# Performance work log

Measured on AMD Instinct MI355X. Metric: run time of the kernel, lower is better.

## Reference

```python
import jax, jax.numpy as jnp
import numpy as np

# ---- static config (from module code / init_kwargs) ----
D_MODEL = 512
D_STATE = 64
D_CONV = 4
EXPAND = 2
HEADDIM = 64
D_INNER = EXPAND * D_MODEL          # 1024
NHEADS = D_INNER // HEADDIM         # 16
D_IN_PROJ = 2 * D_INNER + 2 * D_STATE + NHEADS  # 2192
CONV_DIM = D_INNER + 2 * D_STATE    # 1152
N_LAYERS = 2
VOCAB = 32768
BATCH = 2
SEQ = 512
EPS = 1e-5


def setup_inputs() -> dict:
    key = jax.random.key(0)
    ks = jax.random.split(key, 12)
    g = lambda k, shape, s=0.02: (jax.random.normal(k, shape, jnp.float32) * s)
    return {
        "input_ids": jax.random.randint(ks[0], (BATCH, SEQ), 0, VOCAB),
        "padding_mask": jnp.zeros((BATCH, SEQ), dtype=bool),  # True = pad
        "embeddings": g(ks[1], (VOCAB, D_MODEL)),
        "in_proj_w": g(ks[2], (N_LAYERS, D_IN_PROJ, D_MODEL)),
        "conv_w": g(ks[3], (N_LAYERS, CONV_DIM, D_CONV), 0.1),
        "conv_b": jnp.zeros((N_LAYERS, CONV_DIM), jnp.float32),
        "dt_bias": g(ks[4], (N_LAYERS, NHEADS), 0.5),
        "A_log": jnp.log(jax.random.uniform(ks[5], (N_LAYERS, NHEADS), jnp.float32, 1.0, 16.0)),
        "D_ssm": jnp.ones((N_LAYERS, NHEADS), jnp.float32),
        "norm_w": jnp.ones((N_LAYERS, D_INNER), jnp.float32),
        "out_proj_w": g(ks[6], (N_LAYERS, D_MODEL, D_INNER)),
        "aggr_w": g(ks[7], (D_MODEL, 2 * D_MODEL)),
        "aggr_b": jnp.zeros((D_MODEL,), jnp.float32),
        "norm_f_w": jnp.ones((D_MODEL,), jnp.float32),
        "lm_head_w": g(ks[8], (VOCAB, D_MODEL)),
        "lm_head_b": jnp.zeros((VOCAB,), jnp.float32),
    }


def rmsnorm(x, w):
    return x * jax.lax.rsqrt(jnp.mean(x * x, axis=-1, keepdims=True) + EPS) * w


def flip_sc(X, padding_mask):
    # reverse the valid (non-pad) prefix of each sequence, leave pad positions in place
    b, l, _ = X.shape
    lengths = jnp.sum(~padding_mask, axis=1)                        # (b,)
    pos = jnp.arange(l)[None, :]                                    # (1,l)
    keep = pos < lengths[:, None]
    rev = jnp.where(keep, lengths[:, None] - 1 - pos, pos)          # (b,l)
    return jnp.take_along_axis(X, rev[:, :, None], axis=1)


def causal_conv(x, w, b):
    # x: (b,l,c); depthwise causal conv with kernel size D_CONV
    xt = jnp.transpose(x, (0, 2, 1))                                # (b,c,l)
    y = jax.lax.conv_general_dilated(
        xt, w[:, None, :], window_strides=(1,), padding=[(D_CONV - 1, 0)],
        feature_group_count=w.shape[0], dimension_numbers=("NCH", "OIH", "NCH"))
    return jnp.transpose(y + b[None, :, None], (0, 2, 1))


def ssd_scan(x, dt, A, B, C):
    # x:(b,l,h,p) dt:(b,l,h) A:(h,) B,C:(b,l,n) -> y:(b,l,h,p)
    bsz = x.shape[0]
    dA = jnp.exp(dt * A)                                            # (b,l,h)
    dtx = dt[..., None] * x                                         # (b,l,h,p)
    def step(h, inp):
        dA_t, dtx_t, B_t, C_t = inp
        h = h * dA_t[:, :, None, None] + dtx_t[..., None] * B_t[:, None, None, :]
        y = jnp.einsum("bhpn,bn->bhp", h, C_t)
        return h, y
    h0 = jnp.zeros((bsz, NHEADS, HEADDIM, D_STATE), x.dtype)
    xs = (jnp.swapaxes(dA, 0, 1), jnp.swapaxes(dtx, 0, 1),
          jnp.swapaxes(B, 0, 1), jnp.swapaxes(C, 0, 1))
    _, ys = jax.lax.scan(step, h0, xs)
    return jnp.swapaxes(ys, 0, 1)


def mamba2_block(x, wi, cw, cb, dtb, alog, dss, nw, wo):
    # Mamba2 layer with residual (EncoderLayer: mamba(X) + X)
    b, l, _ = x.shape
    zxbcdt = jnp.einsum("bld,ed->ble", x, wi)                      # (b,l,D_IN_PROJ)
    z = zxbcdt[..., :D_INNER]
    xBC = zxbcdt[..., D_INNER:D_INNER + CONV_DIM]
    dt = jax.nn.softplus(zxbcdt[..., D_INNER + CONV_DIM:] + dtb)   # (b,l,h)
    xBC = jax.nn.silu(causal_conv(xBC, cw, cb))
    xs = xBC[..., :D_INNER].reshape(b, l, NHEADS, HEADDIM)
    B = xBC[..., D_INNER:D_INNER + D_STATE]
    C = xBC[..., D_INNER + D_STATE:]
    A = -jnp.exp(alog)                                             # (h,)
    y = ssd_scan(xs, dt, A, B, C) + xs * dss[None, None, :, None]
    y = y.reshape(b, l, D_INNER)
    y = rmsnorm(y * jax.nn.silu(z), nw)                            # RMSNormGated
    return jnp.einsum("ble,de->bld", y, wo) + x


def reference(input_ids, padding_mask, embeddings, in_proj_w, conv_w, conv_b,
              dt_bias, A_log, D_ssm, norm_w, out_proj_w, aggr_w, aggr_b,
              norm_f_w, lm_head_w, lm_head_b):
    X = embeddings[input_ids]                                      # (b,l,d)
    for i in range(N_LAYERS):
        X_flip = flip_sc(X, padding_mask)
        X_f = mamba2_block(X, in_proj_w[i], conv_w[i], conv_b[i], dt_bias[i],
                           A_log[i], D_ssm[i], norm_w[i], out_proj_w[i])
        X_b = mamba2_block(X_flip, in_proj_w[i], conv_w[i], conv_b[i], dt_bias[i],
                           A_log[i], D_ssm[i], norm_w[i], out_proj_w[i])
        X_b = flip_sc(X_b, padding_mask)
        # gated bidirectional fusion
        zg = jax.nn.sigmoid(jnp.concatenate([X_f, X_b], axis=-1) @ aggr_w.T + aggr_b)
        X = zg * X_f + (1.0 - zg) * X_b
    h = rmsnorm(X, norm_f_w)
    logits = h @ lm_head_w.T + lm_head_b                            # (b,l,V)
    return logits
```

## Files before the change

kernel.cpp:

```cpp
#include <hip/hip_runtime.h>

#define SEQ    512
#define DM     512
#define DI     1024
#define NH     16
#define DS     64
#define CONVD  1152
#define DPROJ  2192
#define NPADIN 2304

typedef __attribute__((ext_vector_type(8))) short bf16x8;
typedef __attribute__((ext_vector_type(4))) float floatx4;

__device__ __forceinline__ unsigned int f2bf(float f) {
  unsigned int u = __float_as_uint(f);
  u += 0x7FFFu + ((u >> 16) & 1u);
  return u >> 16;
}
__device__ __forceinline__ ushort4 cvt4(float4 v) {
  ushort4 o;
  o.x = (unsigned short)f2bf(v.x); o.y = (unsigned short)f2bf(v.y);
  o.z = (unsigned short)f2bf(v.z); o.w = (unsigned short)f2bf(v.w);
  return o;
}
__device__ __forceinline__ float sigmoidf_(float x) { return 1.f / (1.f + __expf(-x)); }
__device__ __forceinline__ float siluf_(float x) { return x * sigmoidf_(x); }

__device__ __forceinline__ void gl16(const void* g, void* l) {
  __builtin_amdgcn_global_load_lds(
      (const __attribute__((address_space(1))) unsigned int*)g,
      (__attribute__((address_space(3))) unsigned int*)l, 16, 0, 0);
}

template<int BM, int BN, int EPI>
__global__ __launch_bounds__(256) void gemm_bf(
    const short* __restrict__ A, const short* __restrict__ B,
    float* __restrict__ C, const int K, const int Nvalid, const int ldc,
    const float* __restrict__ e0, const float* __restrict__ e1,
    unsigned short* __restrict__ o2)
{
  constexpr int FM = BM / 32, FN = BN / 32;
  constexpr int PA = BM / 32, PB = BN / 32;
  __shared__ short As[BM * 64];
  __shared__ short Bs[BN * 64];
  const int tid = threadIdx.x, lane = tid & 63, wave = tid >> 6;
  const int m0 = blockIdx.y * BM, n0 = blockIdx.x * BN;
  const int wm = (wave >> 1) * (BM / 2), wn = (wave & 1) * (BN / 2);
  const int prow = wave * 8 + (lane >> 3);
  const int schk = ((lane & 7) ^ (prow & 7)) << 3;
  const short* agp = A + (size_t)(m0 + prow) * K + schk;
  const short* bgp = B + (size_t)(n0 + prow) * K + schk;
  short* albase = &As[wave * 8 * 64];
  short* blbase = &Bs[wave * 8 * 64];
  const int r16 = lane & 15, quad = lane >> 4;

  floatx4 acc[FM][FN];
#pragma unroll
  for (int i = 0; i < FM; i++)
#pragma unroll
    for (int j = 0; j < FN; j++) acc[i][j] = (floatx4)0.f;

  for (int k0 = 0; k0 < K; k0 += 64) {
#pragma unroll
    for (int p = 0; p < PA; ++p)
      gl16(agp + (size_t)p * 32 * K + k0, albase + p * 32 * 64);
#pragma unroll
    for (int p = 0; p < PB; ++p)
      gl16(bgp + (size_t)p * 32 * K + k0, blbase + p * 32 * 64);
    __syncthreads();
#pragma unroll
    for (int kk = 0; kk < 2; ++kk) {
      bf16x8 afr[FM], bfr[FN];
#pragma unroll
      for (int i = 0; i < FM; i++) {
        const int row = wm + i * 16 + r16;
        afr[i] = *(const bf16x8*)&As[row * 64 + (((kk * 4 + quad) ^ (row & 7)) << 3)];
      }
#pragma unroll
      for (int j = 0; j < FN; j++) {
        const int row = wn + j * 16 + r16;
        bfr[j] = *(const bf16x8*)&Bs[row * 64 + (((kk * 4 + quad) ^ (row & 7)) << 3)];
      }
#pragma unroll
      for (int i = 0; i < FM; i++)
#pragma unroll
        for (int j = 0; j < FN; j++)
          acc[i][j] = __builtin_amdgcn_mfma_f32_16x16x32_bf16(afr[i], bfr[j], acc[i][j], 0, 0, 0);
    }
    __syncthreads();
  }

  const int er = quad << 2;
#pragma unroll
  for (int i = 0; i < FM; ++i)
#pragma unroll
    for (int j = 0; j < FN; ++j)
#pragma unroll
      for (int r = 0; r < 4; ++r) {
        const int gm = m0 + wm + i * 16 + er + r;
        const int gn = n0 + wn + j * 16 + r16;
        float v = acc[i][j][r];
        if (EPI == 0) {
          if (gn < Nvalid) C[(size_t)gm * ldc + gn] = v;
        } else if (EPI == 1) {
          const int mm = gm & 1023;
          v += e0[(size_t)mm * DM + gn];
          const size_t idx = (size_t)mm * DI + ((gm >> 10) << 9) + gn;
          C[idx] = v;
          o2[idx] = (unsigned short)f2bf(v);
        } else if (EPI == 2) {
          const float zg = sigmoidf_(v + e0[gn]);
          const float xn = zg * e1[(size_t)gm * DI + gn] +
                           (1.f - zg) * e1[(size_t)gm * DI + DM + gn];
          const size_t idx = (size_t)gm * DM + gn;
          C[idx] = xn;
          o2[idx] = (unsigned short)f2bf(xn);
        } else {
          C[(size_t)gm * ldc + gn] = v + e0[gn];
        }
      }
}

#define WO4  262144
#define AW4  131072
#define LM4  4194304
__global__ __launch_bounds__(256) void prep_k(
    const int* __restrict__ ids, const float* __restrict__ emb,
    const float* __restrict__ wi, const float* __restrict__ wo,
    const float* __restrict__ aw, const float* __restrict__ lmw,
    float* __restrict__ Xf, unsigned short* __restrict__ Xb,
    unsigned short* __restrict__ wiB, unsigned short* __restrict__ woB,
    unsigned short* __restrict__ awB, unsigned short* __restrict__ lmwB) {
  const int blk = blockIdx.x, tid = threadIdx.x;
  if (blk < 512) {
    const int m = blk * 2 + (tid >> 7), col = tid & 127;
    const int row = ids[m];
    float4 v = ((const float4*)(emb + (size_t)row * DM))[col];
    ((float4*)(Xf + (size_t)m * DM))[col] = v;
    ((ushort4*)(Xb + (size_t)m * DM))[col] = cvt4(v);
  } else if (blk < 512 + 2304) {
    const int slot = (blk - 512) * 2 + (tid >> 7), col = tid & 127;
    const int l = slot >= 2304 ? 1 : 0;
    const int row = slot - l * 2304;
    ushort4 o; o.x = o.y = o.z = o.w = 0;
    if (row < DPROJ)
      o = cvt4(((const float4*)(wi + ((size_t)l * DPROJ + row) * DM))[col]);
    ((ushort4*)(wiB + ((size_t)l * NPADIN + row) * DM))[col] = o;
  } else {
    for (int i = (blk - 2816) * 256 + tid; i < WO4 + AW4 + LM4; i += 4480 * 256) {
      int j = i;
      const float4* s; ushort4* d;
      if (j < WO4)            { s = (const float4*)wo;  d = (ushort4*)woB; }
      else if (j < WO4 + AW4) { j -= WO4; s = (const float4*)aw;  d = (ushort4*)awB; }
      else                    { j -= WO4 + AW4; s = (const float4*)lmw; d = (ushort4*)lmwB; }
      d[j] = cvt4(s[j]);
    }
  }
}

__global__ __launch_bounds__(256) void conv_k(const float* __restrict__ zx,
    const float* __restrict__ cw, const float* __restrict__ cb,
    const float* __restrict__ dtb, const float* __restrict__ alog,
    float* __restrict__ xact, float* __restrict__ dtt, float* __restrict__ dAt) {
  const int t0 = (blockIdx.x & 31) << 4;
  const int half = blockIdx.x >> 5;
  const int b = blockIdx.y;
  const float* src = zx + (size_t)b * SEQ * DPROJ + DI;
  float* d0 = xact + (size_t)b * SEQ * CONVD;
  float* d1 = xact + (size_t)(2 + b) * SEQ * CONVD;

  for (int cc = 0; cc < 3; ++cc) {
    const int ci = cc * 256 + threadIdx.x;
    if (ci >= 576) break;
    const int c = half * 576 + ci;
    const float w0 = cw[c*4+0], w1 = cw[c*4+1], w2 = cw[c*4+2], w3 = cw[c*4+3];
    const float bias = cb[c];
    float a_[22];
#pragma unroll
    for (int j = 0; j < 22; ++j) {
      const int t = t0 - 3 + j;
      a_[j] = (t >= 0 && t < SEQ) ? src[(size_t)t * DPROJ + c] : 0.f;
    }
#pragma unroll
    for (int tt = 0; tt < 16; ++tt) {
      const float f = bias + w0*a_[tt]   + w1*a_[tt+1] + w2*a_[tt+2] + w3*a_[tt+3];
      const float g = bias + w3*a_[tt+3] + w2*a_[tt+4] + w1*a_[tt+5] + w0*a_[tt+6];
      d0[(size_t)(t0+tt) * CONVD + c] = siluf_(f);
      d1[(size_t)(t0+tt) * CONVD + c] = siluf_(g);
    }
  }
  if (half == 0) {
    const int hh = threadIdx.x >> 4, tt2 = threadIdx.x & 15;
    const int t = t0 + tt2;
    const float v = zx[(size_t)(b * SEQ + t) * DPROJ + 2176 + hh] + dtb[hh];
    const float dt = (v > 15.f) ? v : log1pf(__expf(v));
    const float A = -__expf(alog[hh]);
    dtt[(b * NH + hh) * SEQ + t] = dt;
    dAt[(b * NH + hh) * SEQ + t] = __expf(dt * A);
  }
}

__global__ __launch_bounds__(256, 1) void scan_k(const float* __restrict__ xact,
    const float* __restrict__ dtt, const float* __restrict__ dAt,
    float* __restrict__ yn) {
  const int bid = blockIdx.x;
  const int dir = bid >> 7, b = (bid >> 6) & 1, h = (bid >> 2) & 15;
  const int ph = (bid >> 1) & 1, nh = bid & 1;
  const int tid = threadIdx.x, pl = tid & 31, nq = tid >> 5;
  const int p = ph * 32 + pl, nb = nq << 2;
  const float* __restrict__ src = xact + (size_t)(dir * 2 + b) * SEQ * CONVD;
  const float* __restrict__ dtp = dtt + (b * NH + h) * SEQ;
  const float* __restrict__ dap = dAt + (b * NH + h) * SEQ;
  float* __restrict__ yrow = yn + (size_t)nh * (4 * SEQ * DI)
      + (size_t)(dir * 2 + b) * SEQ * DI + h * 64 + ph * 32;
  __shared__ float yp[2][8][16][33];
  float hs[4] = {0.f, 0.f, 0.f, 0.f};
  int pb = 0;

  for (int c0 = 0; c0 < SEQ; c0 += 16, pb ^= 1) {
#pragma unroll
    for (int s = 0; s < 16; ++s) {
      const int tn = dir ? (SEQ - 1 - (c0 + s)) : (c0 + s);
      const float* row = src + (size_t)tn * CONVD;
      const float dts = dtp[tn];
      const float das = dap[tn];
      const float xv = row[h * 64 + p];
      const float4 b4 = *(const float4*)(row + DI + nh * 32 + nb);
      const float4 c4 = *(const float4*)(row + DI + DS + nh * 32 + nb);
      const float dtx = dts * xv;
      float ya;
      hs[0] = hs[0] * das + dtx * b4.x; ya  = hs[0] * c4.x;
      hs[1] = hs[1] * das + dtx * b4.y; ya += hs[1] * c4.y;
      hs[2] = hs[2] * das + dtx * b4.z; ya += hs[2] * c4.z;
      hs[3] = hs[3] * das + dtx * b4.w; ya += hs[3] * c4.w;
      yp[pb][nq][s][pl] = ya;
    }
    __syncthreads();
    {
      const int rt = tid >> 4, rp = (tid & 15) << 1;
      const int tn = dir ? (SEQ - 1 - (c0 + rt)) : (c0 + rt);
      float s0 = 0.f, s1 = 0.f;
#pragma unroll
      for (int j = 0; j < 8; ++j) { s0 += yp[pb][j][rt][rp]; s1 += yp[pb][j][rt][rp + 1]; }
      float2 o; o.x = s0; o.y = s1;
      *(float2*)&yrow[(size_t)tn * DI + rp] = o;
    }
  }
}

__global__ __launch_bounds__(256) void p2_k(const float* __restrict__ yn,
    const float* __restrict__ xact, const float* __restrict__ zx,
    const float* __restrict__ dss, const float* __restrict__ nw,
    unsigned short* __restrict__ A2b) {
  const int m2 = blockIdx.x;
  const int e4 = threadIdx.x << 2;
  const float4 ya = *(const float4*)(yn + (size_t)m2 * DI + e4);
  const float4 yb = *(const float4*)(yn + (size_t)4 * SEQ * DI + (size_t)m2 * DI + e4);
  const float4 x4 = *(const float4*)(xact + (size_t)m2 * CONVD + e4);
  const float4 z4 = *(const float4*)(zx + (size_t)(m2 & 1023) * DPROJ + e4);
  const float d = dss[e4 >> 6];
  float4 g;
  g.x = (ya.x + yb.x + x4.x * d) * siluf_(z4.x);
  g.y = (ya.y + yb.y + x4.y * d) * siluf_(z4.y);
  g.z = (ya.z + yb.z + x4.z * d) * siluf_(z4.z);
  g.w = (ya.w + yb.w + x4.w * d) * siluf_(z4.w);
  float ss = g.x*g.x + g.y*g.y + g.z*g.z + g.w*g.w;
#pragma unroll
  for (int m = 32; m >= 1; m >>= 1) ss += __shfl_xor(ss, m);
  __shared__ float red[4];
  if ((threadIdx.x & 63) == 0) red[threadIdx.x >> 6] = ss;
  __syncthreads();
  const float tot = red[0] + red[1] + red[2] + red[3];
  const float sc = rsqrtf(tot * (1.f / 1024.f) + 1e-5f);
  const float4 w4 = *(const float4*)(nw + e4);
  float4 o;
  o.x = g.x * sc * w4.x; o.y = g.y * sc * w4.y;
  o.z = g.z * sc * w4.z; o.w = g.w * sc * w4.w;
  ((ushort4*)(A2b + (size_t)m2 * DI))[threadIdx.x] = cvt4(o);
}

__global__ __launch_bounds__(128) void fnorm_k(const float* __restrict__ X,
    const float* __restrict__ w, unsigned short* __restrict__ outb) {
  const int m = blockIdx.x;
  const int e4 = threadIdx.x << 2;
  const float4 x4 = *(const float4*)(X + (size_t)m * DM + e4);
  float ss = x4.x*x4.x + x4.y*x4.y + x4.z*x4.z + x4.w*x4.w;
#pragma unroll
  for (int mm = 32; mm >= 1; mm >>= 1) ss += __shfl_xor(ss, mm);
  __shared__ float red[2];
  if ((threadIdx.x & 63) == 0) red[threadIdx.x >> 6] = ss;
  __syncthreads();
  const float tot = red[0] + red[1];
  const float sc = rsqrtf(tot * (1.f / 512.f) + 1e-5f);
  const float4 w4 = *(const float4*)(w + e4);
  float4 o;
  o.x = x4.x * sc * w4.x; o.y = x4.y * sc * w4.y;
  o.z = x4.z * sc * w4.z; o.w = x4.w * sc * w4.w;
  ((ushort4*)(outb + (size_t)m * DM))[threadIdx.x] = cvt4(o);
}

extern "C" void kernel_launch(void* const* d_in, const int* in_sizes, int n_in,
                              void* d_out, int out_size, void* d_ws, size_t ws_size,
                              hipStream_t stream) {
  (void)in_sizes; (void)n_in; (void)out_size; (void)ws_size;
  const int*   ids  = (const int*)d_in[0];
  const float* emb  = (const float*)d_in[2];
  const float* wi   = (const float*)d_in[3];
  const float* cw   = (const float*)d_in[4];
  const float* cb   = (const float*)d_in[5];
  const float* dtb  = (const float*)d_in[6];
  const float* alog = (const float*)d_in[7];
  const float* dss  = (const float*)d_in[8];
  const float* nw   = (const float*)d_in[9];
  const float* wo   = (const float*)d_in[10];
  const float* aw   = (const float*)d_in[11];
  const float* ab   = (const float*)d_in[12];
  const float* nfw  = (const float*)d_in[13];
  const float* lmw  = (const float*)d_in[14];
  const float* lmb  = (const float*)d_in[15];
  float* out = (float*)d_out;

  float* ws    = (float*)d_ws;
  float* Xf    = ws;
  float* zx    = Xf    + (size_t)524288;
  float* xact  = zx    + (size_t)2244608;
  float* dtt   = xact  + (size_t)2359296;
  float* dAt   = dtt   + (size_t)16384;
  float* yn    = dAt   + (size_t)16384;
  float* Xcatf = yn    + (size_t)4194304;
  unsigned short* Xb    = (unsigned short*)(Xcatf + (size_t)1048576);
  unsigned short* A2b   = Xb    + (size_t)524288;
  unsigned short* Xcatb = A2b   + (size_t)2097152;
  unsigned short* hnb   = Xcatb + (size_t)1048576;
  unsigned short* wiB   = hnb   + (size_t)524288;
  unsigned short* woB   = wiB   + (size_t)2359296;
  unsigned short* awB   = woB   + (size_t)1048576;
  unsigned short* lmwB  = awB   + (size_t)524288;

  prep_k<<<dim3(7296), dim3(256), 0, stream>>>(ids, emb, wi, wo, aw, lmw,
                                               Xf, Xb, wiB, woB, awB, lmwB);

  for (int layer = 0; layer < 2; ++layer) {
    gemm_bf<128, 128, 0><<<dim3(18, 8), dim3(256), 0, stream>>>(
        (const short*)Xb, (const short*)(wiB + (size_t)layer * NPADIN * DM),
        zx, 512, 2192, 2192, nullptr, nullptr, nullptr);
    conv_k<<<dim3(64, 2), dim3(256), 0, stream>>>(
        zx, cw + (size_t)layer * 4608, cb + (size_t)layer * 1152,
        dtb + 16 * layer, alog + 16 * layer, xact, dtt, dAt);
    scan_k<<<dim3(256), dim3(256), 0, stream>>>(xact, dtt, dAt, yn);
    p2_k<<<dim3(2048), dim3(256), 0, stream>>>(yn, xact, zx, dss + 16 * layer,
                                               nw + (size_t)layer * 1024, A2b);
    gemm_bf<64, 128, 1><<<dim3(4, 32), dim3(256), 0, stream>>>(
        (const short*)A2b, (const short*)(woB + (size_t)layer * DM * DI),
        Xcatf, 1024, 512, 512, Xf, nullptr, Xcatb);
    gemm_bf<64, 64, 2><<<dim3(8, 16), dim3(256), 0, stream>>>(
        (const short*)Xcatb, (const short*)awB,
        Xf, 1024, 512, 512, ab, Xcatf, Xb);
  }
  fnorm_k<<<dim3(1024), dim3(128), 0, stream>>>(Xf, nfw, hnb);
  gemm_bf<128, 128, 3><<<dim3(256, 8), dim3(256), 0, stream>>>(
      (const short*)hnb, (const short*)lmwB, out, 512, 32768, 32768, lmb, nullptr, nullptr);
}
```

Baseline: 513.7 us.

## Fuse fp32-to-bf16 weight conversion into GEMM B-tile loads, drop weight prep pass

Removes the prep pass that converted all weights (in_proj, out_proj, aggr, lm_head) to bf16 copies in workspace. The GEMM now reads fp32 weight rows directly, converts them with packed bf16 conversion instructions, and stores them into the swizzled shared tile, clamping out-of-range rows instead of relying on zero padding. This avoids writing and re-reading a bf16 weight copy, but doubles the B-operand global read bytes and swaps async global-to-LDS loads for register-staged loads, which may reduce latency hiding, notably in the large lm_head GEMM where each weight tile is re-read by every M block.

After: 550.1 us. 7.1% more time.

```diff
diff --git a/kernel.cpp b/kernel.cpp
--- a/kernel.cpp
+++ b/kernel.cpp
@@ -7,7 +7,6 @@
 #define DS     64
 #define CONVD  1152
 #define DPROJ  2192
-#define NPADIN 2304
 
 typedef __attribute__((ext_vector_type(8))) short bf16x8;
 typedef __attribute__((ext_vector_type(4))) float floatx4;
@@ -23,6 +22,11 @@
   o.z = (unsigned short)f2bf(v.z); o.w = (unsigned short)f2bf(v.w);
   return o;
 }
+__device__ __forceinline__ unsigned int cvtpk(float lo, float hi) {
+  unsigned int r;
+  asm("v_cvt_pk_bf16_f32 %0, %1, %2" : "=v"(r) : "v"(lo), "v"(hi));
+  return r;
+}
 __device__ __forceinline__ float sigmoidf_(float x) { return 1.f / (1.f + __expf(-x)); }
 __device__ __forceinline__ float siluf_(float x) { return x * sigmoidf_(x); }
 
@@ -34,7 +38,7 @@
 
 template<int BM, int BN, int EPI>
 __global__ __launch_bounds__(256) void gemm_bf(
-    const short* __restrict__ A, const short* __restrict__ B,
+    const short* __restrict__ A, const float* __restrict__ B,
     float* __restrict__ C, const int K, const int Nvalid, const int ldc,
     const float* __restrict__ e0, const float* __restrict__ e1,
     unsigned short* __restrict__ o2)
@@ -49,9 +53,7 @@
   const int prow = wave * 8 + (lane >> 3);
   const int schk = ((lane & 7) ^ (prow & 7)) << 3;
   const short* agp = A + (size_t)(m0 + prow) * K + schk;
-  const short* bgp = B + (size_t)(n0 + prow) * K + schk;
   short* albase = &As[wave * 8 * 64];
-  short* blbase = &Bs[wave * 8 * 64];
   const int r16 = lane & 15, quad = lane >> 4;
 
   floatx4 acc[FM][FN];
@@ -65,8 +67,17 @@
     for (int p = 0; p < PA; ++p)
       gl16(agp + (size_t)p * 32 * K + k0, albase + p * 32 * 64);
 #pragma unroll
-    for (int p = 0; p < PB; ++p)
-      gl16(bgp + (size_t)p * 32 * K + k0, blbase + p * 32 * 64);
+    for (int p = 0; p < PB; ++p) {
+      int brow = n0 + p * 32 + prow;
+      brow = (brow < Nvalid) ? brow : (Nvalid - 1);
+      const float* src = B + (size_t)brow * K + k0 + schk;
+      const float4 f0 = *(const float4*)(src);
+      const float4 f1 = *(const float4*)(src + 4);
+      int4 w;
+      w.x = (int)cvtpk(f0.x, f0.y); w.y = (int)cvtpk(f0.z, f0.w);
+      w.z = (int)cvtpk(f1.x, f1.y); w.w = (int)cvtpk(f1.z, f1.w);
+      *(int4*)&Bs[wave * 512 + p * 2048 + lane * 8] = w;
+    }
     __syncthreads();
 #pragma unroll
     for (int kk = 0; kk < 2; ++kk) {
@@ -121,41 +132,14 @@
       }
 }
 
-#define WO4  262144
-#define AW4  131072
-#define LM4  4194304
 __global__ __launch_bounds__(256) void prep_k(
     const int* __restrict__ ids, const float* __restrict__ emb,
-    const float* __restrict__ wi, const float* __restrict__ wo,
-    const float* __restrict__ aw, const float* __restrict__ lmw,
-    float* __restrict__ Xf, unsigned short* __restrict__ Xb,
-    unsigned short* __restrict__ wiB, unsigned short* __restrict__ woB,
-    unsigned short* __restrict__ awB, unsigned short* __restrict__ lmwB) {
-  const int blk = blockIdx.x, tid = threadIdx.x;
-  if (blk < 512) {
-    const int m = blk * 2 + (tid >> 7), col = tid & 127;
-    const int row = ids[m];
-    float4 v = ((const float4*)(emb + (size_t)row * DM))[col];
-    ((float4*)(Xf + (size_t)m * DM))[col] = v;
-    ((ushort4*)(Xb + (size_t)m * DM))[col] = cvt4(v);
-  } else if (blk < 512 + 2304) {
-    const int slot = (blk - 512) * 2 + (tid >> 7), col = tid & 127;
-    const int l = slot >= 2304 ? 1 : 0;
-    const int row = slot - l * 2304;
-    ushort4 o; o.x = o.y = o.z = o.w = 0;
-    if (row < DPROJ)
-      o = cvt4(((const float4*)(wi + ((size_t)l * DPROJ + row) * DM))[col]);
-    ((ushort4*)(wiB + ((size_t)l * NPADIN + row) * DM))[col] = o;
-  } else {
-    for (int i = (blk - 2816) * 256 + tid; i < WO4 + AW4 + LM4; i += 4480 * 256) {
-      int j = i;
-      const float4* s; ushort4* d;
-      if (j < WO4)            { s = (const float4*)wo;  d = (ushort4*)woB; }
-      else if (j < WO4 + AW4) { j -= WO4; s = (const float4*)aw;  d = (ushort4*)awB; }
-      else                    { j -= WO4 + AW4; s = (const float4*)lmw; d = (ushort4*)lmwB; }
-      d[j] = cvt4(s[j]);
-    }
-  }
+    float* __restrict__ Xf, unsigned short* __restrict__ Xb) {
+  const int m = blockIdx.x * 2 + (threadIdx.x >> 7), col = threadIdx.x & 127;
+  const int row = ids[m];
+  float4 v = ((const float4*)(emb + (size_t)row * DM))[col];
+  ((float4*)(Xf + (size_t)m * DM))[col] = v;
+  ((ushort4*)(Xb + (size_t)m * DM))[col] = cvt4(v);
 }
 
 __global__ __launch_bounds__(256) void conv_k(const float* __restrict__ zx,
@@ -332,17 +316,12 @@
   unsigned short* A2b   = Xb    + (size_t)524288;
   unsigned short* Xcatb = A2b   + (size_t)2097152;
   unsigned short* hnb   = Xcatb + (size_t)1048576;
-  unsigned short* wiB   = hnb   + (size_t)524288;
-  unsigned short* woB   = wiB   + (size_t)2359296;
-  unsigned short* awB   = woB   + (size_t)1048576;
-  unsigned short* lmwB  = awB   + (size_t)524288;
-
-  prep_k<<<dim3(7296), dim3(256), 0, stream>>>(ids, emb, wi, wo, aw, lmw,
-                                               Xf, Xb, wiB, woB, awB, lmwB);
+
+  prep_k<<<dim3(512), dim3(256), 0, stream>>>(ids, emb, Xf, Xb);
 
   for (int layer = 0; layer < 2; ++layer) {
     gemm_bf<128, 128, 0><<<dim3(18, 8), dim3(256), 0, stream>>>(
-        (const short*)Xb, (const short*)(wiB + (size_t)layer * NPADIN * DM),
+        (const short*)Xb, wi + (size_t)layer * DPROJ * DM,
         zx, 512, 2192, 2192, nullptr, nullptr, nullptr);
     conv_k<<<dim3(64, 2), dim3(256), 0, stream>>>(
         zx, cw + (size_t)layer * 4608, cb + (size_t)layer * 1152,
@@ -351,13 +330,13 @@
     p2_k<<<dim3(2048), dim3(256), 0, stream>>>(yn, xact, zx, dss + 16 * layer,
                                                nw + (size_t)layer * 1024, A2b);
     gemm_bf<64, 128, 1><<<dim3(4, 32), dim3(256), 0, stream>>>(
-        (const short*)A2b, (const short*)(woB + (size_t)layer * DM * DI),
+        (const short*)A2b, wo + (size_t)layer * DM * DI,
         Xcatf, 1024, 512, 512, Xf, nullptr, Xcatb);
     gemm_bf<64, 64, 2><<<dim3(8, 16), dim3(256), 0, stream>>>(
-        (const short*)Xcatb, (const short*)awB,
+        (const short*)Xcatb, aw,
         Xf, 1024, 512, 512, ab, Xcatf, Xb);
   }
   fnorm_k<<<dim3(1024), dim3(128), 0, stream>>>(Xf, nfw, hnb);
   gemm_bf<128, 128, 3><<<dim3(256, 8), dim3(256), 0, stream>>>(
-      (const short*)hnb, (const short*)lmwB, out, 512, 32768, 32768, lmb, nullptr, nullptr);
-}
+      (const short*)hnb, lmw, out, 512, 32768, 32768, lmb, nullptr, nullptr);
+}
```

## Double-buffer GEMM LDS tiles and XCD-swizzle LM-head block mapping

Applied to the files above, without the earlier changes.

The bf16 MFMA GEMM now uses two LDS buffers per operand, so the global-to-LDS load of the next K tile is issued before computing the current one, with one barrier per half-step. The intent is to hide global load latency behind MFMA work. The LM-head GEMM also moves to a 1D grid whose block index is remapped so that blocks on the same XCD share B (weight) column tiles and all 8 M tiles, aiming for better L2 reuse. Doubling LDS per block may lower occupancy, and the remap assumes 8 XCDs and exactly 2048 blocks.

After: 518.6 us. About the same (+1.0%).

```diff
diff --git a/kernel.cpp b/kernel.cpp
--- a/kernel.cpp
+++ b/kernel.cpp
@@ -32,7 +32,7 @@
       (__attribute__((address_space(3))) unsigned int*)l, 16, 0, 0);
 }
 
-template<int BM, int BN, int EPI>
+template<int BM, int BN, int EPI, int XSWZ>
 __global__ __launch_bounds__(256) void gemm_bf(
     const short* __restrict__ A, const short* __restrict__ B,
     float* __restrict__ C, const int K, const int Nvalid, const int ldc,
@@ -41,17 +41,25 @@
 {
   constexpr int FM = BM / 32, FN = BN / 32;
   constexpr int PA = BM / 32, PB = BN / 32;
-  __shared__ short As[BM * 64];
-  __shared__ short Bs[BN * 64];
+  __shared__ short As0[BM * 64];
+  __shared__ short As1[BM * 64];
+  __shared__ short Bs0[BN * 64];
+  __shared__ short Bs1[BN * 64];
   const int tid = threadIdx.x, lane = tid & 63, wave = tid >> 6;
-  const int m0 = blockIdx.y * BM, n0 = blockIdx.x * BN;
+  int m0, n0;
+  if (XSWZ) {
+    const int wg = blockIdx.x;
+    const int xcd = wg & 7, local = wg >> 3;
+    m0 = (local & 7) * BM;
+    n0 = ((xcd << 5) | (local >> 3)) * BN;
+  } else {
+    m0 = blockIdx.y * BM; n0 = blockIdx.x * BN;
+  }
   const int wm = (wave >> 1) * (BM / 2), wn = (wave & 1) * (BN / 2);
   const int prow = wave * 8 + (lane >> 3);
   const int schk = ((lane & 7) ^ (prow & 7)) << 3;
   const short* agp = A + (size_t)(m0 + prow) * K + schk;
   const short* bgp = B + (size_t)(n0 + prow) * K + schk;
-  short* albase = &As[wave * 8 * 64];
-  short* blbase = &Bs[wave * 8 * 64];
   const int r16 = lane & 15, quad = lane >> 4;
 
   floatx4 acc[FM][FN];
@@ -60,35 +68,52 @@
 #pragma unroll
     for (int j = 0; j < FN; j++) acc[i][j] = (floatx4)0.f;
 
-  for (int k0 = 0; k0 < K; k0 += 64) {
-#pragma unroll
-    for (int p = 0; p < PA; ++p)
-      gl16(agp + (size_t)p * 32 * K + k0, albase + p * 32 * 64);
-#pragma unroll
-    for (int p = 0; p < PB; ++p)
-      gl16(bgp + (size_t)p * 32 * K + k0, blbase + p * 32 * 64);
+#define STAGE(k0, ASB, BSB) do {                                              \
+    _Pragma("unroll")                                                         \
+    for (int p = 0; p < PA; ++p)                                              \
+      gl16(agp + (size_t)p * 32 * K + (k0), (ASB) + wave * 512 + p * 2048);   \
+    _Pragma("unroll")                                                         \
+    for (int p = 0; p < PB; ++p)                                              \
+      gl16(bgp + (size_t)p * 32 * K + (k0), (BSB) + wave * 512 + p * 2048);   \
+  } while (0)
+
+#define COMPUTE(ASB, BSB) do {                                                \
+    _Pragma("unroll")                                                         \
+    for (int kk = 0; kk < 2; ++kk) {                                          \
+      bf16x8 afr[FM], bfr[FN];                                                \
+      _Pragma("unroll")                                                       \
+      for (int i = 0; i < FM; i++) {                                          \
+        const int row = wm + i * 16 + r16;                                    \
+        afr[i] = *(const bf16x8*)&(ASB)[row * 64 +                            \
+                 (((kk * 4 + quad) ^ (row & 7)) << 3)];                       \
+      }                                                                       \
+      _Pragma("unroll")                                                       \
+      for (int j = 0; j < FN; j++) {                                          \
+        const int row = wn + j * 16 + r16;                                    \
+        bfr[j] = *(const bf16x8*)&(BSB)[row * 64 +                            \
+                 (((kk * 4 + quad) ^ (row & 7)) << 3)];                       \
+      }                                                                       \
+      _Pragma("unroll")                                                       \
+      for (int i = 0; i < FM; i++)                                            \
+        _Pragma("unroll")                                                     \
+        for (int j = 0; j < FN; j++)                                          \
+          acc[i][j] = __builtin_amdgcn_mfma_f32_16x16x32_bf16(                \
+              afr[i], bfr[j], acc[i][j], 0, 0, 0);                            \
+    }                                                                         \
+  } while (0)
+
+  STAGE(0, As0, Bs0);
+  __syncthreads();
+  for (int k0 = 0; k0 < K; k0 += 128) {
+    STAGE(k0 + 64, As1, Bs1);
+    COMPUTE(As0, Bs0);
     __syncthreads();
-#pragma unroll
-    for (int kk = 0; kk < 2; ++kk) {
-      bf16x8 afr[FM], bfr[FN];
-#pragma unroll
-      for (int i = 0; i < FM; i++) {
-        const int row = wm + i * 16 + r16;
-        afr[i] = *(const bf16x8*)&As[row * 64 + (((kk * 4 + quad) ^ (row & 7)) << 3)];
-      }
-#pragma unroll
-      for (int j = 0; j < FN; j++) {
-        const int row = wn + j * 16 + r16;
-        bfr[j] = *(const bf16x8*)&Bs[row * 64 + (((kk * 4 + quad) ^ (row & 7)) << 3)];
-      }
-#pragma unroll
-      for (int i = 0; i < FM; i++)
-#pragma unroll
-        for (int j = 0; j < FN; j++)
-          acc[i][j] = __builtin_amdgcn_mfma_f32_16x16x32_bf16(afr[i], bfr[j], acc[i][j], 0, 0, 0);
-    }
+    if (k0 + 128 < K) STAGE(k0 + 128, As0, Bs0);
+    COMPUTE(As1, Bs1);
     __syncthreads();
   }
+#undef STAGE
+#undef COMPUTE
 
   const int er = quad << 2;
 #pragma unroll
@@ -341,7 +366,7 @@
                                                Xf, Xb, wiB, woB, awB, lmwB);
 
   for (int layer = 0; layer < 2; ++layer) {
-    gemm_bf<128, 128, 0><<<dim3(18, 8), dim3(256), 0, stream>>>(
+    gemm_bf<128, 128, 0, 0><<<dim3(18, 8), dim3(256), 0, stream>>>(
         (const short*)Xb, (const short*)(wiB + (size_t)layer * NPADIN * DM),
         zx, 512, 2192, 2192, nullptr, nullptr, nullptr);
     conv_k<<<dim3(64, 2), dim3(256), 0, stream>>>(
@@ -350,14 +375,15 @@
     scan_k<<<dim3(256), dim3(256), 0, stream>>>(xact, dtt, dAt, yn);
     p2_k<<<dim3(2048), dim3(256), 0, stream>>>(yn, xact, zx, dss + 16 * layer,
                                                nw + (size_t)layer * 1024, A2b);
-    gemm_bf<64, 128, 1><<<dim3(4, 32), dim3(256), 0, stream>>>(
+    gemm_bf<64, 128, 1, 0><<<dim3(4, 32), dim3(256), 0, stream>>>(
         (const short*)A2b, (const short*)(woB + (size_t)layer * DM * DI),
         Xcatf, 1024, 512, 512, Xf, nullptr, Xcatb);
-    gemm_bf<64, 64, 2><<<dim3(8, 16), dim3(256), 0, stream>>>(
+    gemm_bf<64, 64, 2, 0><<<dim3(8, 16), dim3(256), 0, stream>>>(
         (const short*)Xcatb, (const short*)awB,
         Xf, 1024, 512, 512, ab, Xcatf, Xb);
   }
   fnorm_k<<<dim3(1024), dim3(128), 0, stream>>>(Xf, nfw, hnb);
-  gemm_bf<128, 128, 3><<<dim3(256, 8), dim3(256), 0, stream>>>(
-      (const short*)hnb, (const short*)lmwB, out, 512, 32768, 32768, lmb, nullptr, nullptr);
-}
+  gemm_bf<128, 128, 3, 1><<<dim3(2048), dim3(256), 0, stream>>>(
+      (const short*)hnb, (const short*)lmwB, out, 512, 32768, 32768, lmb,
+      nullptr, nullptr);
+}
```

## Split scan, conv and small GEMMs finer; add XCD-aware swizzle to lm_head GEMM

Applied to the files above, without the earlier changes.

The scan kernel now uses 512 blocks, each owning 16 head-dim lanes and 2 state elements per thread, with a 16-way shared-memory reduction. It also drops the single-block-per-CU launch bound. The conv kernel processes 8 timesteps per block instead of 16, doubling its grid. The in_proj, out_proj and aggregation GEMMs use smaller tiles (64x64 and 32x64) to launch more workgroups. The final lm_head GEMM remaps its 1D block id so that the 8 M-tiles sharing a weight tile land on the same XCD, to improve L2 reuse. The aim is better occupancy for the latency-bound small kernels, at the cost of more redundant loads and more reduction work in the scan.

Result: slower. 563.0 us (+9.6%).

```diff
diff --git a/kernel.cpp b/kernel.cpp
--- a/kernel.cpp
+++ b/kernel.cpp
@@ -32,7 +32,7 @@
       (__attribute__((address_space(3))) unsigned int*)l, 16, 0, 0);
 }
 
-template<int BM, int BN, int EPI>
+template<int BM, int BN, int EPI, int XSWZ>
 __global__ __launch_bounds__(256) void gemm_bf(
     const short* __restrict__ A, const short* __restrict__ B,
     float* __restrict__ C, const int K, const int Nvalid, const int ldc,
@@ -40,18 +40,26 @@
     unsigned short* __restrict__ o2)
 {
   constexpr int FM = BM / 32, FN = BN / 32;
-  constexpr int PA = BM / 32, PB = BN / 32;
+  constexpr int PA = (BM + 31) / 32, PB = BN / 32;
   __shared__ short As[BM * 64];
   __shared__ short Bs[BN * 64];
   const int tid = threadIdx.x, lane = tid & 63, wave = tid >> 6;
-  const int m0 = blockIdx.y * BM, n0 = blockIdx.x * BN;
+  int m0, n0;
+  if (XSWZ) {
+    const int wg = blockIdx.x;
+    const int xcd = wg & 7, local = wg >> 3;
+    m0 = (local & 7) * BM;
+    n0 = ((xcd << 5) | (local >> 3)) * BN;
+  } else {
+    m0 = blockIdx.y * BM; n0 = blockIdx.x * BN;
+  }
   const int wm = (wave >> 1) * (BM / 2), wn = (wave & 1) * (BN / 2);
   const int prow = wave * 8 + (lane >> 3);
   const int schk = ((lane & 7) ^ (prow & 7)) << 3;
   const short* agp = A + (size_t)(m0 + prow) * K + schk;
   const short* bgp = B + (size_t)(n0 + prow) * K + schk;
-  short* albase = &As[wave * 8 * 64];
-  short* blbase = &Bs[wave * 8 * 64];
+  short* albase = &As[wave * 512];
+  short* blbase = &Bs[wave * 512];
   const int r16 = lane & 15, quad = lane >> 4;
 
   floatx4 acc[FM][FN];
@@ -63,10 +71,10 @@
   for (int k0 = 0; k0 < K; k0 += 64) {
 #pragma unroll
     for (int p = 0; p < PA; ++p)
-      gl16(agp + (size_t)p * 32 * K + k0, albase + p * 32 * 64);
+      gl16(agp + (size_t)p * 32 * K + k0, albase + p * 2048);
 #pragma unroll
     for (int p = 0; p < PB; ++p)
-      gl16(bgp + (size_t)p * 32 * K + k0, blbase + p * 32 * 64);
+      gl16(bgp + (size_t)p * 32 * K + k0, blbase + p * 2048);
     __syncthreads();
 #pragma unroll
     for (int kk = 0; kk < 2; ++kk) {
@@ -162,8 +170,8 @@
     const float* __restrict__ cw, const float* __restrict__ cb,
     const float* __restrict__ dtb, const float* __restrict__ alog,
     float* __restrict__ xact, float* __restrict__ dtt, float* __restrict__ dAt) {
-  const int t0 = (blockIdx.x & 31) << 4;
-  const int half = blockIdx.x >> 5;
+  const int t0 = (blockIdx.x & 63) << 3;
+  const int half = blockIdx.x >> 6;
   const int b = blockIdx.y;
   const float* src = zx + (size_t)b * SEQ * DPROJ + DI;
   float* d0 = xact + (size_t)b * SEQ * CONVD;
@@ -175,22 +183,22 @@
     const int c = half * 576 + ci;
     const float w0 = cw[c*4+0], w1 = cw[c*4+1], w2 = cw[c*4+2], w3 = cw[c*4+3];
     const float bias = cb[c];
-    float a_[22];
-#pragma unroll
-    for (int j = 0; j < 22; ++j) {
+    float a_[14];
+#pragma unroll
+    for (int j = 0; j < 14; ++j) {
       const int t = t0 - 3 + j;
       a_[j] = (t >= 0 && t < SEQ) ? src[(size_t)t * DPROJ + c] : 0.f;
     }
 #pragma unroll
-    for (int tt = 0; tt < 16; ++tt) {
+    for (int tt = 0; tt < 8; ++tt) {
       const float f = bias + w0*a_[tt]   + w1*a_[tt+1] + w2*a_[tt+2] + w3*a_[tt+3];
       const float g = bias + w3*a_[tt+3] + w2*a_[tt+4] + w1*a_[tt+5] + w0*a_[tt+6];
       d0[(size_t)(t0+tt) * CONVD + c] = siluf_(f);
       d1[(size_t)(t0+tt) * CONVD + c] = siluf_(g);
     }
   }
-  if (half == 0) {
-    const int hh = threadIdx.x >> 4, tt2 = threadIdx.x & 15;
+  if (half == 0 && threadIdx.x < 128) {
+    const int hh = threadIdx.x >> 3, tt2 = threadIdx.x & 7;
     const int t = t0 + tt2;
     const float v = zx[(size_t)(b * SEQ + t) * DPROJ + 2176 + hh] + dtb[hh];
     const float dt = (v > 15.f) ? v : log1pf(__expf(v));
@@ -200,21 +208,21 @@
   }
 }
 
-__global__ __launch_bounds__(256, 1) void scan_k(const float* __restrict__ xact,
+__global__ __launch_bounds__(256) void scan_k(const float* __restrict__ xact,
     const float* __restrict__ dtt, const float* __restrict__ dAt,
     float* __restrict__ yn) {
   const int bid = blockIdx.x;
-  const int dir = bid >> 7, b = (bid >> 6) & 1, h = (bid >> 2) & 15;
-  const int ph = (bid >> 1) & 1, nh = bid & 1;
-  const int tid = threadIdx.x, pl = tid & 31, nq = tid >> 5;
-  const int p = ph * 32 + pl, nb = nq << 2;
+  const int dir = bid >> 8, b = (bid >> 7) & 1, h = (bid >> 3) & 15;
+  const int ph = (bid >> 1) & 3, nh = bid & 1;
+  const int tid = threadIdx.x, pl = tid & 15, nq = tid >> 4;
+  const int p = ph * 16 + pl, nb = nq << 1;
   const float* __restrict__ src = xact + (size_t)(dir * 2 + b) * SEQ * CONVD;
   const float* __restrict__ dtp = dtt + (b * NH + h) * SEQ;
   const float* __restrict__ dap = dAt + (b * NH + h) * SEQ;
   float* __restrict__ yrow = yn + (size_t)nh * (4 * SEQ * DI)
-      + (size_t)(dir * 2 + b) * SEQ * DI + h * 64 + ph * 32;
-  __shared__ float yp[2][8][16][33];
-  float hs[4] = {0.f, 0.f, 0.f, 0.f};
+      + (size_t)(dir * 2 + b) * SEQ * DI + h * 64 + ph * 16;
+  __shared__ float yp[2][16][16][17];
+  float hs[2] = {0.f, 0.f};
   int pb = 0;
 
   for (int c0 = 0; c0 < SEQ; c0 += 16, pb ^= 1) {
@@ -225,25 +233,22 @@
       const float dts = dtp[tn];
       const float das = dap[tn];
       const float xv = row[h * 64 + p];
-      const float4 b4 = *(const float4*)(row + DI + nh * 32 + nb);
-      const float4 c4 = *(const float4*)(row + DI + DS + nh * 32 + nb);
+      const float2 b2 = *(const float2*)(row + DI + nh * 32 + nb);
+      const float2 c2 = *(const float2*)(row + DI + DS + nh * 32 + nb);
       const float dtx = dts * xv;
       float ya;
-      hs[0] = hs[0] * das + dtx * b4.x; ya  = hs[0] * c4.x;
-      hs[1] = hs[1] * das + dtx * b4.y; ya += hs[1] * c4.y;
-      hs[2] = hs[2] * das + dtx * b4.z; ya += hs[2] * c4.z;
-      hs[3] = hs[3] * das + dtx * b4.w; ya += hs[3] * c4.w;
+      hs[0] = hs[0] * das + dtx * b2.x; ya  = hs[0] * c2.x;
+      hs[1] = hs[1] * das + dtx * b2.y; ya += hs[1] * c2.y;
       yp[pb][nq][s][pl] = ya;
     }
     __syncthreads();
     {
-      const int rt = tid >> 4, rp = (tid & 15) << 1;
+      const int rt = tid >> 4, rp = tid & 15;
       const int tn = dir ? (SEQ - 1 - (c0 + rt)) : (c0 + rt);
-      float s0 = 0.f, s1 = 0.f;
-#pragma unroll
-      for (int j = 0; j < 8; ++j) { s0 += yp[pb][j][rt][rp]; s1 += yp[pb][j][rt][rp + 1]; }
-      float2 o; o.x = s0; o.y = s1;
-      *(float2*)&yrow[(size_t)tn * DI + rp] = o;
+      float s0 = 0.f;
+#pragma unroll
+      for (int j = 0; j < 16; ++j) s0 += yp[pb][j][rt][rp];
+      yrow[(size_t)tn * DI + rp] = s0;
     }
   }
 }
@@ -341,23 +346,24 @@
                                                Xf, Xb, wiB, woB, awB, lmwB);
 
   for (int layer = 0; layer < 2; ++layer) {
-    gemm_bf<128, 128, 0><<<dim3(18, 8), dim3(256), 0, stream>>>(
+    gemm_bf<64, 64, 0, 0><<<dim3(36, 16), dim3(256), 0, stream>>>(
         (const short*)Xb, (const short*)(wiB + (size_t)layer * NPADIN * DM),
         zx, 512, 2192, 2192, nullptr, nullptr, nullptr);
-    conv_k<<<dim3(64, 2), dim3(256), 0, stream>>>(
+    conv_k<<<dim3(128, 2), dim3(256), 0, stream>>>(
         zx, cw + (size_t)layer * 4608, cb + (size_t)layer * 1152,
         dtb + 16 * layer, alog + 16 * layer, xact, dtt, dAt);
-    scan_k<<<dim3(256), dim3(256), 0, stream>>>(xact, dtt, dAt, yn);
+    scan_k<<<dim3(512), dim3(256), 0, stream>>>(xact, dtt, dAt, yn);
     p2_k<<<dim3(2048), dim3(256), 0, stream>>>(yn, xact, zx, dss + 16 * layer,
                                                nw + (size_t)layer * 1024, A2b);
-    gemm_bf<64, 128, 1><<<dim3(4, 32), dim3(256), 0, stream>>>(
+    gemm_bf<64, 64, 1, 0><<<dim3(8, 32), dim3(256), 0, stream>>>(
         (const short*)A2b, (const short*)(woB + (size_t)layer * DM * DI),
         Xcatf, 1024, 512, 512, Xf, nullptr, Xcatb);
-    gemm_bf<64, 64, 2><<<dim3(8, 16), dim3(256), 0, stream>>>(
+    gemm_bf<32, 64, 2, 0><<<dim3(8, 32), dim3(256), 0, stream>>>(
         (const short*)Xcatb, (const short*)awB,
         Xf, 1024, 512, 512, ab, Xcatf, Xb);
   }
   fnorm_k<<<dim3(1024), dim3(128), 0, stream>>>(Xf, nfw, hnb);
-  gemm_bf<128, 128, 3><<<dim3(256, 8), dim3(256), 0, stream>>>(
-      (const short*)hnb, (const short*)lmwB, out, 512, 32768, 32768, lmb, nullptr, nullptr);
-}
+  gemm_bf<128, 128, 3, 1><<<dim3(2048), dim3(256), 0, stream>>>(
+      (const short*)hnb, (const short*)lmwB, out, 512, 32768, 32768, lmb,
+      nullptr, nullptr);
+}
```
